# Kernel optimization log

Hardware: AMD Instinct MI355X
Metric: run time of the kernel (lower is better)

## Reference

```python
import jax, jax.numpy as jnp
import numpy as np

B, T, D = 1, 2048, 1024
H = 16
SEM_DIM, GEO_DIM, ATTN_DIM = 512, 512, 1024
ROPE_BASE = 10000.0
NEG = -1e9


def setup_inputs() -> dict:
    key = jax.random.key(0)
    ks = jax.random.split(key, 10)
    s = 0.02
    return {
        "x": jax.random.normal(ks[0], (B, T, D), jnp.float32),
        "wq_sem": jax.random.normal(ks[1], (D, SEM_DIM), jnp.float32) * s,
        "wk_sem": jax.random.normal(ks[2], (D, SEM_DIM), jnp.float32) * s,
        "wq_geo": jax.random.normal(ks[3], (D, GEO_DIM), jnp.float32) * s,
        "wk_geo": jax.random.normal(ks[4], (D, GEO_DIM), jnp.float32) * s,
        "wv": jax.random.normal(ks[5], (D, ATTN_DIM), jnp.float32) * s,
        "wo": jax.random.normal(ks[6], (ATTN_DIM, D), jnp.float32) * s,
        "k_sem_null": jax.random.normal(ks[7], (SEM_DIM,), jnp.float32) * s,
        "k_geo_null": jax.random.normal(ks[8], (GEO_DIM,), jnp.float32) * s,
        "v_null": jax.random.normal(ks[9], (ATTN_DIM,), jnp.float32) * s,
    }


def _heads(y, hd):
    b, t, _ = y.shape
    return y.reshape(b, t, H, hd).transpose(0, 2, 1, 3)  # [B,H,T,hd]


def _rope(x, cos, sin):
    # x: [B,H,T,hd], cos/sin: [T,hd//2] (rotate-half convention)
    hd = x.shape[-1]
    x1, x2 = x[..., : hd // 2], x[..., hd // 2 :]
    c = cos[None, None]
    sn = sin[None, None]
    return jnp.concatenate([x1 * c - x2 * sn, x2 * c + x1 * sn], axis=-1)


def _forward(x, wq_sem, wk_sem, wq_geo, wk_geo, wv, wo, k_sem_null, k_geo_null, v_null):
    b, t, _ = x.shape
    sem_hd = wq_sem.shape[1] // H
    geo_hd = wq_geo.shape[1] // H
    v_hd = wv.shape[1] // H
    sem_scale = 1.0 / np.sqrt(sem_hd)
    geo_scale = 1.0 / np.sqrt(geo_hd)

    qs = _heads(x @ wq_sem, sem_hd)
    ks = _heads(x @ wk_sem, sem_hd)
    qg = _heads(x @ wq_geo, geo_hd)
    kg = _heads(x @ wk_geo, geo_hd)
    v = _heads(x @ wv, v_hd)

    # RoPE on geometric branch only
    pos = jnp.arange(t, dtype=jnp.float32)
    inv_freq = 1.0 / (ROPE_BASE ** (jnp.arange(0, geo_hd, 2, dtype=jnp.float32) / geo_hd))
    ang = pos[:, None] * inv_freq[None, :]  # [T, geo_hd//2]
    cos, sin = jnp.cos(ang), jnp.sin(ang)
    qg = _rope(qg, cos, sin)
    kg = _rope(kg, cos, sin)

    # prepend null KV slot (not rotated, always attendable)
    ksn = jnp.broadcast_to(k_sem_null.reshape(1, 1, H, sem_hd).transpose(0, 2, 1, 3), (b, H, 1, sem_hd))
    kgn = jnp.broadcast_to(k_geo_null.reshape(1, 1, H, geo_hd).transpose(0, 2, 1, 3), (b, H, 1, geo_hd))
    vn = jnp.broadcast_to(v_null.reshape(1, 1, H, v_hd).transpose(0, 2, 1, 3), (b, H, 1, v_hd))
    ks_full = jnp.concatenate([ksn, ks], axis=2)  # [B,H,T+1,sem_hd]
    kg_full = jnp.concatenate([kgn, kg], axis=2)
    v_full = jnp.concatenate([vn, v], axis=2)

    # decoupled scores in fp32: sem*sem_scale + geo*geo_scale
    scores = (
        jnp.einsum("bhqd,bhkd->bhqk", qs, ks_full).astype(jnp.float32) * sem_scale
        + jnp.einsum("bhqd,bhkd->bhqk", qg, kg_full).astype(jnp.float32) * geo_scale
    )

    # causal mask over real tokens; null slot (key index 0) always visible
    causal = jnp.tril(jnp.ones((t, t), dtype=bool))
    mask = jnp.concatenate([jnp.ones((t, 1), dtype=bool), causal], axis=1)  # [T, T+1]
    scores = jnp.where(mask[None, None], scores, NEG)

    probs = jax.nn.softmax(scores, axis=-1).astype(v.dtype)
    out = jnp.einsum("bhqk,bhkd->bhqd", probs, v_full)  # [B,H,T,v_hd]
    out = out.transpose(0, 2, 1, 3).reshape(b, t, H * v_hd)
    return out @ wo


def reference(x, wq_sem, wk_sem, wq_geo, wk_geo, wv, wo, k_sem_null, k_geo_null, v_null):
    return _forward(x, wq_sem, wk_sem, wq_geo, wk_geo, wv, wo, k_sem_null, k_geo_null, v_null)
```

## Files before the change

kernel.cpp:

```cpp
#include <hip/hip_runtime.h>
#include <hip/hip_bf16.h>

typedef __hip_bfloat16 bf16;
typedef __attribute__((ext_vector_type(8))) short bf16x8;
typedef __attribute__((ext_vector_type(4))) short bf16x4;
typedef __attribute__((ext_vector_type(4))) float f32x4;

#define TSEQ   2048
#define DMODEL 1024
#define NHEAD  16
#define KST    2112
#define SCALE  0.17677669529663687f
#define LN1E4_16 0.5756462732485115f

__device__ __forceinline__ unsigned short f2bf(float f) {
    union { bf16 h; unsigned short u; } x;
    x.h = __float2bfloat16(f);
    return x.u;
}
__device__ __forceinline__ float bf2f(unsigned short u) {
    return __uint_as_float(((unsigned int)u) << 16);
}

__device__ __forceinline__ void gload_lds16(const void* g, void* l) {
    __builtin_amdgcn_global_load_lds(
        (const __attribute__((address_space(1))) void*)g,
        (__attribute__((address_space(3))) void*)l, 16, 0, 0);
}

__global__ __launch_bounds__(256) void convert_x(const float* __restrict__ X,
                                                 unsigned short* __restrict__ Xb)
{
    int i = (blockIdx.x * 256 + threadIdx.x) * 4;
    float4 v = *(const float4*)(X + i);
    ushort4 o;
    o.x = f2bf(v.x); o.y = f2bf(v.y); o.z = f2bf(v.z); o.w = f2bf(v.w);
    *(ushort4*)(Xb + i) = o;
}

__global__ __launch_bounds__(256) void transpose_all(
    const float* __restrict__ wqs, const float* __restrict__ wks,
    const float* __restrict__ wqg, const float* __restrict__ wkg,
    const float* __restrict__ wv,  const float* __restrict__ wo,
    unsigned short* __restrict__ WcatT, unsigned short* __restrict__ WoT)
{
    __shared__ float T[64][65];
    const float* src; unsigned short* dst; int C;
    switch (blockIdx.z) {
        case 0: src = wqs; dst = WcatT;               C = 512;  break;
        case 1: src = wks; dst = WcatT + 512  * 1024; C = 512;  break;
        case 2: src = wqg; dst = WcatT + 1024 * 1024; C = 512;  break;
        case 3: src = wkg; dst = WcatT + 1536 * 1024; C = 512;  break;
        case 4: src = wv;  dst = WcatT + 2048 * 1024; C = 1024; break;
        default: src = wo; dst = WoT;                 C = 1024; break;
    }
    const int c0 = blockIdx.x * 64;
    if (c0 >= C) return;
    const int r0 = blockIdx.y * 64;
    const int tid = threadIdx.x;
    #pragma unroll
    for (int i = 0; i < 16; ++i) {
        int idx = tid + 256 * i;
        int r = idx >> 6, c = idx & 63;
        T[r][c] = src[(size_t)(r0 + r) * C + c0 + c];
    }
    __syncthreads();
    #pragma unroll
    for (int i = 0; i < 16; ++i) {
        int idx = tid + 256 * i;
        int cc = idx >> 6, rr = idx & 63;
        dst[(size_t)(c0 + cc) * 1024 + r0 + rr] = f2bf(T[rr][cc]);
    }
}

__global__ __launch_bounds__(256) void init_null(
    const float* __restrict__ ksn, const float* __restrict__ kgn,
    const float* __restrict__ vn,
    unsigned short* __restrict__ Kc, unsigned short* __restrict__ Vg)
{
    const int h = blockIdx.x;
    const int tid = threadIdx.x;
    const int d = tid & 63, g = tid >> 6;
    if (g == 0)
        Kc[((size_t)h * KST + 0) * 64 + d] =
            f2bf(d < 32 ? ksn[h * 32 + d] : kgn[h * 32 + d - 32]);
    if (g == 1)
        Vg[((size_t)h * 64 + d) * KST + 0] = f2bf(vn[h * 64 + d]);
    for (int fk = 2049 + g; fk < KST; fk += 4) {
        Kc[((size_t)h * KST + fk) * 64 + d] = 0;
        Vg[((size_t)h * 64 + d) * KST + fk] = 0;
    }
}

__global__ __launch_bounds__(256) void gemm_proj_fused(
    const unsigned short* __restrict__ A,
    const unsigned short* __restrict__ Bt,
    unsigned short* __restrict__ Qc,
    unsigned short* __restrict__ Kc,
    unsigned short* __restrict__ Vg)
{
    __shared__ __align__(16) unsigned short Abuf[64 * 32];
    __shared__ __align__(16) unsigned short Bbuf[128 * 32];
    const int n0 = blockIdx.x * 128, m0 = blockIdx.y * 64;
    const int tid = threadIdx.x, l = tid & 63, wv = tid >> 6;
    const int wr = wv >> 1, wc = wv & 1;
    const int lr = l & 15, lg = l >> 4, kf = lg * 8;

    const int arow = wv * 16 + (l >> 2);
    const int aseg = (l & 3) * 8;

    f32x4 acc[2][4];
    #pragma unroll
    for (int i = 0; i < 2; ++i)
        #pragma unroll
        for (int j = 0; j < 4; ++j) acc[i][j] = (f32x4){0.f, 0.f, 0.f, 0.f};

    for (int k0 = 0; k0 < 1024; k0 += 32) {
        gload_lds16(A + (size_t)(m0 + arow) * 1024 + k0 + aseg, &Abuf[wv * 512]);
        #pragma unroll
        for (int it = 0; it < 2; ++it) {
            int brow = it * 64 + wv * 16 + (l >> 2);
            gload_lds16(Bt + (size_t)(n0 + brow) * 1024 + k0 + aseg,
                        &Bbuf[(it * 256 + wv * 64) * 8]);
        }
        __syncthreads();
        bf16x8 af[2], bfv[4];
        #pragma unroll
        for (int mf = 0; mf < 2; ++mf)
            af[mf] = *(const bf16x8*)&Abuf[(wr * 32 + mf * 16 + lr) * 32 + kf];
        #pragma unroll
        for (int nf = 0; nf < 4; ++nf)
            bfv[nf] = *(const bf16x8*)&Bbuf[(wc * 64 + nf * 16 + lr) * 32 + kf];
        #pragma unroll
        for (int mf = 0; mf < 2; ++mf)
            #pragma unroll
            for (int nf = 0; nf < 4; ++nf)
                acc[mf][nf] = __builtin_amdgcn_mfma_f32_16x16x32_bf16(
                    af[mf], bfv[nf], acc[mf][nf], 0, 0, 0);
        __syncthreads();
    }

    const int sec = n0 >> 9;
    if (sec <= 1) {
        unsigned short* dst = (sec == 0) ? Qc : Kc;
        const int tstr  = (sec == 0) ? TSEQ : KST;
        const int fkoff = (sec == 0) ? 0 : 1;
        const float sc  = (sec == 0) ? SCALE : 1.0f;
        #pragma unroll
        for (int mf = 0; mf < 2; ++mf)
            #pragma unroll
            for (int nf = 0; nf < 4; ++nf) {
                int col = (n0 & 511) + wc * 64 + nf * 16 + lr;
                int h = col >> 5, d = col & 31;
                #pragma unroll
                for (int reg = 0; reg < 4; ++reg) {
                    int q = m0 + wr * 32 + mf * 16 + lg * 4 + reg;
                    dst[((size_t)h * tstr + q + fkoff) * 64 + d] =
                        f2bf(acc[mf][nf][reg] * sc);
                }
            }
    } else if (sec <= 3) {
        unsigned short* dst = (sec == 2) ? Qc : Kc;
        const int tstr  = (sec == 2) ? TSEQ : KST;
        const int fkoff = (sec == 2) ? 0 : 1;
        const float sc  = (sec == 2) ? SCALE : 1.0f;
        const float invf = __expf(-(float)lr * LN1E4_16);
        #pragma unroll
        for (int mf = 0; mf < 2; ++mf)
            #pragma unroll
            for (int reg = 0; reg < 4; ++reg) {
                int q = m0 + wr * 32 + mf * 16 + lg * 4 + reg;
                float s, c;
                __sincosf((float)q * invf, &s, &c);
                #pragma unroll
                for (int nfp = 0; nfp < 2; ++nfp) {
                    int nf0 = nfp * 2;
                    int colbase = (n0 & 511) + wc * 64 + nf0 * 16;
                    int h = colbase >> 5;
                    float x1 = acc[mf][nf0][reg], x2 = acc[mf][nf0 + 1][reg];
                    size_t base = ((size_t)h * tstr + q + fkoff) * 64 + 32;
                    dst[base + lr]      = f2bf((x1 * c - x2 * s) * sc);
                    dst[base + lr + 16] = f2bf((x2 * c + x1 * s) * sc);
                }
            }
    } else {
        #pragma unroll
        for (int nf = 0; nf < 4; ++nf) {
            int colr = (n0 - 2048) + wc * 64 + nf * 16 + lr;
            int h = colr >> 6, dv = colr & 63;
            size_t rowbase = ((size_t)h * 64 + dv) * KST;
            #pragma unroll
            for (int mf = 0; mf < 2; ++mf)
                #pragma unroll
                for (int reg = 0; reg < 4; ++reg) {
                    int q = m0 + wr * 32 + mf * 16 + lg * 4 + reg;
                    Vg[rowbase + q + 1] = f2bf(acc[mf][nf][reg]);
                }
        }
    }
}

__global__ __launch_bounds__(256) void gemm_out(const unsigned short* __restrict__ A,
                                                const unsigned short* __restrict__ Bt,
                                                float* __restrict__ C)
{
    __shared__ __align__(16) unsigned short Abuf[64 * 32];
    __shared__ __align__(16) unsigned short Bbuf[64 * 32];
    const int n0 = blockIdx.x * 64, m0 = blockIdx.y * 64;
    const int tid = threadIdx.x, l = tid & 63, wv = tid >> 6;
    const int wr = wv >> 1, wc = wv & 1;
    const int lr = l & 15, lg = l >> 4, kf = lg * 8;

    const int arow = wv * 16 + (l >> 2);
    const int aseg = (l & 3) * 8;

    f32x4 acc[2][2];
    #pragma unroll
    for (int i = 0; i < 2; ++i)
        #pragma unroll
        for (int j = 0; j < 2; ++j) acc[i][j] = (f32x4){0.f, 0.f, 0.f, 0.f};

    for (int k0 = 0; k0 < 1024; k0 += 32) {
        gload_lds16(A  + (size_t)(m0 + arow) * 1024 + k0 + aseg, &Abuf[wv * 512]);
        gload_lds16(Bt + (size_t)(n0 + arow) * 1024 + k0 + aseg, &Bbuf[wv * 512]);
        __syncthreads();
        bf16x8 af[2], bfv[2];
        #pragma unroll
        for (int mf = 0; mf < 2; ++mf)
            af[mf] = *(const bf16x8*)&Abuf[(wr * 32 + mf * 16 + lr) * 32 + kf];
        #pragma unroll
        for (int nf = 0; nf < 2; ++nf)
            bfv[nf] = *(const bf16x8*)&Bbuf[(wc * 32 + nf * 16 + lr) * 32 + kf];
        #pragma unroll
        for (int mf = 0; mf < 2; ++mf)
            #pragma unroll
            for (int nf = 0; nf < 2; ++nf)
                acc[mf][nf] = __builtin_amdgcn_mfma_f32_16x16x32_bf16(
                    af[mf], bfv[nf], acc[mf][nf], 0, 0, 0);
        __syncthreads();
    }
    #pragma unroll
    for (int mf = 0; mf < 2; ++mf)
        #pragma unroll
        for (int nf = 0; nf < 2; ++nf)
            #pragma unroll
            for (int reg = 0; reg < 4; ++reg) {
                int row = m0 + wr * 32 + mf * 16 + lg * 4 + reg;
                int col = n0 + wc * 32 + nf * 16 + lr;
                C[(size_t)row * DMODEL + col] = acc[mf][nf][reg];
            }
}

__global__ __launch_bounds__(256) void attn_mfma(
    const unsigned short* __restrict__ Qc,
    const unsigned short* __restrict__ Kc,
    const unsigned short* __restrict__ Vg,
    unsigned short* __restrict__ attnO,
    unsigned short* __restrict__ OpA,
    unsigned short* __restrict__ OpB,
    float2* __restrict__ ml)
{
    __shared__ __align__(16) unsigned short KsL[2][64 * 64];
    __shared__ __align__(16) unsigned short VsL[2][64 * 64];
    __shared__ __align__(16) unsigned short Ps[64 * 64];

    const int h = blockIdx.y;
    int qb, part, np;
    {
        int i = blockIdx.x;
        if (i < 24)      { np = 4; qb = 31 - (i >> 2); part = i & 3; }
        else if (i < 51) { int j = i - 24; np = 3; qb = 25 - j / 3; part = j % 3; }
        else if (i < 69) { int j = i - 51; np = 2; qb = 16 - (j >> 1); part = j & 1; }
        else             { np = 1; qb = 7 - (blockIdx.x - 69); part = 0; }
    }
    const int nt = qb + 2;
    const int base = nt / np, rem = nt % np;
    const int t0 = part * base + (part < rem ? part : rem);
    const int t1 = t0 + base + (part < rem ? 1 : 0);

    const int q0 = qb * 64;
    const int tid = threadIdx.x, l = tid & 63, w = tid >> 6;
    const int lr = l & 15, lg = l >> 4;

    const int qrow = q0 + w * 16 + lr;
    bf16x8 qa0 = *(const bf16x8*)&Qc[((size_t)h * TSEQ + qrow) * 64 + lg * 8];
    bf16x8 qa1 = *(const bf16x8*)&Qc[((size_t)h * TSEQ + qrow) * 64 + 32 + lg * 8];

    const int sc8 = (((l & 7) ^ ((l >> 3) & 7))) * 8;
    const int r0s = (w * 2 + 0) * 8 + (l >> 3);
    const int r1s = (w * 2 + 1) * 8 + (l >> 3);
    const unsigned short* Kh = Kc + (((size_t)h * KST) << 6);
    const unsigned short* Vh = Vg + (size_t)h * 64 * KST;

#define STAGE_KV(bufi, fk0_) do {                                              \
        gload_lds16(Kh + (((size_t)((fk0_) + r0s)) << 6) + sc8,                \
                    &KsL[bufi][(w * 2 + 0) * 512]);                            \
        gload_lds16(Kh + (((size_t)((fk0_) + r1s)) << 6) + sc8,                \
                    &KsL[bufi][(w * 2 + 1) * 512]);                            \
        gload_lds16(Vh + (size_t)r0s * KST + (fk0_) + sc8,                     \
                    &VsL[bufi][(w * 2 + 0) * 512]);                            \
        gload_lds16(Vh + (size_t)r1s * KST + (fk0_) + sc8,                     \
                    &VsL[bufi][(w * 2 + 1) * 512]);                            \
    } while (0)

    f32x4 o[4];
    #pragma unroll
    for (int i = 0; i < 4; ++i) o[i] = (f32x4){0.f, 0.f, 0.f, 0.f};
    float m = -1e30f, ll = 0.0f;
    const int q = qrow;

    int buf = 0;
    STAGE_KV(0, t0 * 64);
    asm volatile("s_waitcnt vmcnt(0)" ::: "memory");
    __builtin_amdgcn_s_barrier();

    for (int kb = t0; kb < t1; ++kb) {
        const int fk0 = kb * 64;
        if (kb + 1 < t1) STAGE_KV(buf ^ 1, fk0 + 64);

        const unsigned short* Ksb = &KsL[buf][0];
        const unsigned short* Vsb = &VsL[buf][0];

        f32x4 sa[4];
        #pragma unroll
        for (int i = 0; i < 4; ++i) sa[i] = (f32x4){0.f, 0.f, 0.f, 0.f};
        __builtin_amdgcn_s_setprio(1);
        #pragma unroll
        for (int ks = 0; ks < 2; ++ks) {
            int dd = lg * 8 + ks * 32;
            bf16x8 qa = ks ? qa1 : qa0;
            #pragma unroll
            for (int nf = 0; nf < 4; ++nf) {
                int kkc = nf * 16 + lr;
                bf16x8 kbf = *(const bf16x8*)&Ksb[kkc * 64 + (dd ^ ((kkc & 7) << 3))];
                sa[nf] = __builtin_amdgcn_mfma_f32_16x16x32_bf16(kbf, qa, sa[nf], 0, 0, 0);
            }
        }
        __builtin_amdgcn_s_setprio(0);

        float sv[4][4];
        float mt = -1e30f;
        #pragma unroll
        for (int nf = 0; nf < 4; ++nf)
            #pragma unroll
            for (int reg = 0; reg < 4; ++reg) {
                int fk = fk0 + nf * 16 + lg * 4 + reg;
                float val = (fk <= q + 1) ? sa[nf][reg] : -1e9f;
                sv[nf][reg] = val;
                mt = fmaxf(mt, val);
            }
        mt = fmaxf(mt, __shfl_xor(mt, 16, 64));
        mt = fmaxf(mt, __shfl_xor(mt, 32, 64));
        if (__any(mt > m + 8.0f)) {
            float mn = fmaxf(m, mt);
            float alpha = __expf(m - mn);
            m = mn;
            ll *= alpha;
            #pragma unroll
            for (int nf = 0; nf < 4; ++nf)
                #pragma unroll
                for (int reg = 0; reg < 4; ++reg)
                    o[nf][reg] *= alpha;
        }
        float rs = 0.0f;
        #pragma unroll
        for (int nf = 0; nf < 4; ++nf)
            #pragma unroll
            for (int reg = 0; reg < 4; ++reg) {
                float p = __expf(sv[nf][reg] - m);
                sv[nf][reg] = p;
                rs += p;
            }
        rs += __shfl_xor(rs, 16, 64);
        rs += __shfl_xor(rs, 32, 64);
        ll += rs;

        {
            int r = w * 16 + lr;
            #pragma unroll
            for (int nf = 0; nf < 4; ++nf) {
                bf16x4 pk;
                pk[0] = f2bf(sv[nf][0]); pk[1] = f2bf(sv[nf][1]);
                pk[2] = f2bf(sv[nf][2]); pk[3] = f2bf(sv[nf][3]);
                int kk0 = nf * 16 + lg * 4;
                *(bf16x4*)&Ps[r * 64 + (kk0 ^ ((r & 7) << 3))] = pk;
            }
        }

        __builtin_amdgcn_s_setprio(1);
        #pragma unroll
        for (int ks = 0; ks < 2; ++ks) {
            int kk0 = lg * 8 + ks * 32;
            int pr  = w * 16 + lr;
            bf16x8 pa = *(const bf16x8*)&Ps[pr * 64 + (kk0 ^ ((pr & 7) << 3))];
            #pragma unroll
            for (int nf = 0; nf < 4; ++nf) {
                int dv = nf * 16 + lr;
                bf16x8 vb = *(const bf16x8*)&Vsb[dv * 64 + (kk0 ^ ((dv & 7) << 3))];
                o[nf] = __builtin_amdgcn_mfma_f32_16x16x32_bf16(vb, pa, o[nf], 0, 0, 0);
            }
        }
        __builtin_amdgcn_s_setprio(0);

        asm volatile("s_waitcnt vmcnt(0)" ::: "memory");
        __builtin_amdgcn_s_barrier();
        buf ^= 1;
    }
#undef STAGE_KV

    const float inv = 1.0f / ll;
    if (np == 1) {
        #pragma unroll
        for (int nf = 0; nf < 4; ++nf)
            #pragma unroll
            for (int reg = 0; reg < 4; ++reg) {
                int dv = nf * 16 + lg * 4 + reg;
                attnO[(size_t)q * DMODEL + h * 64 + dv] = f2bf(o[nf][reg] * inv);
            }
    } else {
        const int sidx = h * 69 + blockIdx.x;
        unsigned short* Od = (sidx < 768)
            ? OpA + (size_t)sidx * 4096
            : OpB + (size_t)(sidx - 768) * 4096;
        const int r = w * 16 + lr;
        #pragma unroll
        for (int nf = 0; nf < 4; ++nf)
            #pragma unroll
            for (int reg = 0; reg < 4; ++reg) {
                int dv = nf * 16 + lg * 4 + reg;
                Od[r * 64 + dv] = f2bf(o[nf][reg] * inv);
            }
        if (lg == 0)
            ml[sidx * 64 + r] = make_float2(m, ll);
    }
}

__global__ __launch_bounds__(256) void combine_wave(
    const unsigned short* __restrict__ OpA,
    const unsigned short* __restrict__ OpB,
    const float2* __restrict__ ml,
    unsigned short* __restrict__ attnO)
{
    const int qb = 8 + blockIdx.x;
    const int h  = blockIdx.y;
    int np, i0;
    if (qb >= 26)      { np = 4; i0 = (31 - qb) * 4; }
    else if (qb >= 17) { np = 3; i0 = 24 + (25 - qb) * 3; }
    else               { np = 2; i0 = 51 + (16 - qb) * 2; }
    const int sidx0 = h * 69 + i0;

    const int t = threadIdx.x;
    const int r = t >> 2, dv0 = (t & 3) * 16;

    float wt[4];
    float mm = -1e30f;
    #pragma unroll
    for (int p = 0; p < 4; ++p) {
        wt[p] = 0.0f;
        if (p < np) {
            float2 v = ml[(sidx0 + p) * 64 + r];
            wt[p] = v.x;
            mm = fmaxf(mm, v.x);
        }
    }
    float tot = 0.0f;
    #pragma unroll
    for (int p = 0; p < 4; ++p) {
        if (p < np) {
            float2 v = ml[(sidx0 + p) * 64 + r];
            wt[p] = v.y * __expf(v.x - mm);
            tot += wt[p];
        }
    }
    const float inv = 1.0f / tot;

    float accv[16];
    #pragma unroll
    for (int c = 0; c < 16; ++c) accv[c] = 0.0f;
    #pragma unroll
    for (int p = 0; p < 4; ++p) {
        if (p < np) {
            int s = sidx0 + p;
            const unsigned short* Od = (s < 768)
                ? OpA + (size_t)s * 4096
                : OpB + (size_t)(s - 768) * 4096;
            #pragma unroll
            for (int c4 = 0; c4 < 4; ++c4) {
                ushort4 v = *(const ushort4*)&Od[r * 64 + dv0 + c4 * 4];
                accv[c4 * 4 + 0] += wt[p] * bf2f(v.x);
                accv[c4 * 4 + 1] += wt[p] * bf2f(v.y);
                accv[c4 * 4 + 2] += wt[p] * bf2f(v.z);
                accv[c4 * 4 + 3] += wt[p] * bf2f(v.w);
            }
        }
    }
    const int q = qb * 64 + r;
    #pragma unroll
    for (int c4 = 0; c4 < 4; ++c4) {
        ushort4 ov;
        ov.x = f2bf(accv[c4 * 4 + 0] * inv);
        ov.y = f2bf(accv[c4 * 4 + 1] * inv);
        ov.z = f2bf(accv[c4 * 4 + 2] * inv);
        ov.w = f2bf(accv[c4 * 4 + 3] * inv);
        *(ushort4*)&attnO[(size_t)q * DMODEL + h * 64 + dv0 + c4 * 4] = ov;
    }
}

extern "C" void kernel_launch(void* const* d_in, const int* in_sizes, int n_in,
                              void* d_out, int out_size, void* d_ws, size_t ws_size,
                              hipStream_t stream)
{
    const float* x      = (const float*)d_in[0];
    const float* wq_sem = (const float*)d_in[1];
    const float* wk_sem = (const float*)d_in[2];
    const float* wq_geo = (const float*)d_in[3];
    const float* wk_geo = (const float*)d_in[4];
    const float* wv     = (const float*)d_in[5];
    const float* wo     = (const float*)d_in[6];
    const float* ksn    = (const float*)d_in[7];
    const float* kgn    = (const float*)d_in[8];
    const float* vn     = (const float*)d_in[9];
    float* out = (float*)d_out;

    char* ws = (char*)d_ws;
    unsigned short* Xb    = (unsigned short*)(ws);
    unsigned short* attnO = (unsigned short*)(ws);
    unsigned short* WcatT = (unsigned short*)(ws + 4194304);
    unsigned short* OpA   = (unsigned short*)(ws + 4194304);
    unsigned short* WoT   = (unsigned short*)(ws + 10485760);
    unsigned short* Qc    = (unsigned short*)(ws + 12582912);
    unsigned short* Kc    = (unsigned short*)(ws + 16777216);
    unsigned short* Vg    = (unsigned short*)(ws + 21102592);
    unsigned short* OpB   = (unsigned short*)(ws + 25427968);
    float2*         ml    = (float2*)(ws + 28180480);

    convert_x<<<2048, 256, 0, stream>>>(x, Xb);
    transpose_all<<<dim3(16, 16, 6), 256, 0, stream>>>(
        wq_sem, wk_sem, wq_geo, wk_geo, wv, wo, WcatT, WoT);
    init_null<<<16, 256, 0, stream>>>(ksn, kgn, vn, Kc, Vg);

    gemm_proj_fused<<<dim3(24, 32), 256, 0, stream>>>(Xb, WcatT, Qc, Kc, Vg);

    attn_mfma<<<dim3(77, NHEAD), 256, 0, stream>>>(Qc, Kc, Vg, attnO, OpA, OpB, ml);
    combine_wave<<<dim3(24, NHEAD), 256, 0, stream>>>(OpA, OpB, ml, attnO);

    gemm_out<<<dim3(16, 32), 256, 0, stream>>>(attnO, WoT, out);
}
```

Baseline: 95.32 us.

## Use 128-row query tiles in attention and merge prep kernels into one launch

Attention blocks now cover 128 query rows instead of 64, with each wave computing two 16-row groups against the same K/V tile held in LDS. This halves K/V staging per query row and doubles MFMA work per LDS read. The split-K partition table, partial-output layout, and combine kernel are resized to match. Full causal-mask evaluation is skipped for tiles entirely below the diagonal, and the three preprocessing kernels are merged into a single launch. The trade-off is more register pressure and fewer blocks in the grid.

```diff
diff --git a/kernel.cpp b/kernel.cpp
--- a/kernel.cpp
+++ b/kernel.cpp
@@ -28,67 +28,67 @@
         (__attribute__((address_space(3))) void*)l, 16, 0, 0);
 }
 
-__global__ __launch_bounds__(256) void convert_x(const float* __restrict__ X,
-                                                 unsigned short* __restrict__ Xb)
-{
-    int i = (blockIdx.x * 256 + threadIdx.x) * 4;
-    float4 v = *(const float4*)(X + i);
-    ushort4 o;
-    o.x = f2bf(v.x); o.y = f2bf(v.y); o.z = f2bf(v.z); o.w = f2bf(v.w);
-    *(ushort4*)(Xb + i) = o;
-}
-
-__global__ __launch_bounds__(256) void transpose_all(
+__global__ __launch_bounds__(256) void prep_all(
+    const float* __restrict__ X,
     const float* __restrict__ wqs, const float* __restrict__ wks,
     const float* __restrict__ wqg, const float* __restrict__ wkg,
     const float* __restrict__ wv,  const float* __restrict__ wo,
-    unsigned short* __restrict__ WcatT, unsigned short* __restrict__ WoT)
+    const float* __restrict__ ksn, const float* __restrict__ kgn,
+    const float* __restrict__ vn,
+    unsigned short* __restrict__ Xb,
+    unsigned short* __restrict__ WcatT, unsigned short* __restrict__ WoT,
+    unsigned short* __restrict__ Kc, unsigned short* __restrict__ Vg)
 {
     __shared__ float T[64][65];
-    const float* src; unsigned short* dst; int C;
-    switch (blockIdx.z) {
-        case 0: src = wqs; dst = WcatT;               C = 512;  break;
-        case 1: src = wks; dst = WcatT + 512  * 1024; C = 512;  break;
-        case 2: src = wqg; dst = WcatT + 1024 * 1024; C = 512;  break;
-        case 3: src = wkg; dst = WcatT + 1536 * 1024; C = 512;  break;
-        case 4: src = wv;  dst = WcatT + 2048 * 1024; C = 1024; break;
-        default: src = wo; dst = WoT;                 C = 1024; break;
-    }
-    const int c0 = blockIdx.x * 64;
-    if (c0 >= C) return;
-    const int r0 = blockIdx.y * 64;
+    const int bx = blockIdx.x;
     const int tid = threadIdx.x;
-    #pragma unroll
-    for (int i = 0; i < 16; ++i) {
-        int idx = tid + 256 * i;
-        int r = idx >> 6, c = idx & 63;
-        T[r][c] = src[(size_t)(r0 + r) * C + c0 + c];
-    }
-    __syncthreads();
-    #pragma unroll
-    for (int i = 0; i < 16; ++i) {
-        int idx = tid + 256 * i;
-        int cc = idx >> 6, rr = idx & 63;
-        dst[(size_t)(c0 + cc) * 1024 + r0 + rr] = f2bf(T[rr][cc]);
-    }
-}
-
-__global__ __launch_bounds__(256) void init_null(
-    const float* __restrict__ ksn, const float* __restrict__ kgn,
-    const float* __restrict__ vn,
-    unsigned short* __restrict__ Kc, unsigned short* __restrict__ Vg)
-{
-    const int h = blockIdx.x;
-    const int tid = threadIdx.x;
-    const int d = tid & 63, g = tid >> 6;
-    if (g == 0)
-        Kc[((size_t)h * KST + 0) * 64 + d] =
-            f2bf(d < 32 ? ksn[h * 32 + d] : kgn[h * 32 + d - 32]);
-    if (g == 1)
-        Vg[((size_t)h * 64 + d) * KST + 0] = f2bf(vn[h * 64 + d]);
-    for (int fk = 2049 + g; fk < KST; fk += 4) {
-        Kc[((size_t)h * KST + fk) * 64 + d] = 0;
-        Vg[((size_t)h * 64 + d) * KST + fk] = 0;
+    if (bx < 2048) {
+        int i = (bx * 256 + tid) * 4;
+        float4 v = *(const float4*)(X + i);
+        ushort4 o;
+        o.x = f2bf(v.x); o.y = f2bf(v.y); o.z = f2bf(v.z); o.w = f2bf(v.w);
+        *(ushort4*)(Xb + i) = o;
+    } else if (bx < 3584) {
+        const int idx = bx - 2048;
+        const int z = idx >> 8, rem = idx & 255;
+        const int cx = rem & 15, ry = rem >> 4;
+        const float* src; unsigned short* dst; int C;
+        switch (z) {
+            case 0: src = wqs; dst = WcatT;               C = 512;  break;
+            case 1: src = wks; dst = WcatT + 512  * 1024; C = 512;  break;
+            case 2: src = wqg; dst = WcatT + 1024 * 1024; C = 512;  break;
+            case 3: src = wkg; dst = WcatT + 1536 * 1024; C = 512;  break;
+            case 4: src = wv;  dst = WcatT + 2048 * 1024; C = 1024; break;
+            default: src = wo; dst = WoT;                 C = 1024; break;
+        }
+        const int c0 = cx * 64;
+        if (c0 >= C) return;
+        const int r0 = ry * 64;
+        #pragma unroll
+        for (int i = 0; i < 16; ++i) {
+            int id2 = tid + 256 * i;
+            int r = id2 >> 6, c = id2 & 63;
+            T[r][c] = src[(size_t)(r0 + r) * C + c0 + c];
+        }
+        __syncthreads();
+        #pragma unroll
+        for (int i = 0; i < 16; ++i) {
+            int id2 = tid + 256 * i;
+            int cc = id2 >> 6, rr = id2 & 63;
+            dst[(size_t)(c0 + cc) * 1024 + r0 + rr] = f2bf(T[rr][cc]);
+        }
+    } else {
+        const int h = bx - 3584;
+        const int d = tid & 63, g = tid >> 6;
+        if (g == 0)
+            Kc[((size_t)h * KST + 0) * 64 + d] =
+                f2bf(d < 32 ? ksn[h * 32 + d] : kgn[h * 32 + d - 32]);
+        if (g == 1)
+            Vg[((size_t)h * 64 + d) * KST + 0] = f2bf(vn[h * 64 + d]);
+        for (int fk = 2049 + g; fk < KST; fk += 4) {
+            Kc[((size_t)h * KST + fk) * 64 + d] = 0;
+            Vg[((size_t)h * 64 + d) * KST + fk] = 0;
+        }
     }
 }
 
@@ -262,29 +262,33 @@
 {
     __shared__ __align__(16) unsigned short KsL[2][64 * 64];
     __shared__ __align__(16) unsigned short VsL[2][64 * 64];
-    __shared__ __align__(16) unsigned short Ps[64 * 64];
+    __shared__ __align__(16) unsigned short Ps[128 * 64];
 
     const int h = blockIdx.y;
     int qb, part, np;
     {
         int i = blockIdx.x;
-        if (i < 24)      { np = 4; qb = 31 - (i >> 2); part = i & 3; }
-        else if (i < 51) { int j = i - 24; np = 3; qb = 25 - j / 3; part = j % 3; }
-        else if (i < 69) { int j = i - 51; np = 2; qb = 16 - (j >> 1); part = j & 1; }
-        else             { np = 1; qb = 7 - (blockIdx.x - 69); part = 0; }
-    }
-    const int nt = qb + 2;
-    const int base = nt / np, rem = nt % np;
-    const int t0 = part * base + (part < rem ? part : rem);
-    const int t1 = t0 + base + (part < rem ? 1 : 0);
-
-    const int q0 = qb * 64;
+        if (i < 16)      { np = 4; qb = 15 - (i >> 2); part = i & 3; }
+        else if (i < 28) { int j = i - 16; np = 3; qb = 11 - j / 3; part = j % 3; }
+        else if (i < 38) { int j = i - 28; np = 2; qb = 7 - (j >> 1); part = j & 1; }
+        else             { np = 1; qb = 2 - (blockIdx.x - 38); part = 0; }
+    }
+    const int nt = 2 * qb + 3;
+    const int bsz = nt / np, rem = nt % np;
+    const int t0 = part * bsz + (part < rem ? part : rem);
+    const int t1 = t0 + bsz + (part < rem ? 1 : 0);
+
+    const int q0 = qb * 128;
     const int tid = threadIdx.x, l = tid & 63, w = tid >> 6;
     const int lr = l & 15, lg = l >> 4;
 
-    const int qrow = q0 + w * 16 + lr;
-    bf16x8 qa0 = *(const bf16x8*)&Qc[((size_t)h * TSEQ + qrow) * 64 + lg * 8];
-    bf16x8 qa1 = *(const bf16x8*)&Qc[((size_t)h * TSEQ + qrow) * 64 + 32 + lg * 8];
+    bf16x8 qa[2][2];
+    #pragma unroll
+    for (int rg = 0; rg < 2; ++rg) {
+        int qr = q0 + w * 32 + rg * 16 + lr;
+        qa[rg][0] = *(const bf16x8*)&Qc[((size_t)h * TSEQ + qr) * 64 + lg * 8];
+        qa[rg][1] = *(const bf16x8*)&Qc[((size_t)h * TSEQ + qr) * 64 + 32 + lg * 8];
+    }
 
     const int sc8 = (((l & 7) ^ ((l >> 3) & 7))) * 8;
     const int r0s = (w * 2 + 0) * 8 + (l >> 3);
@@ -303,11 +307,13 @@
                     &VsL[bufi][(w * 2 + 1) * 512]);                            \
     } while (0)
 
-    f32x4 o[4];
-    #pragma unroll
-    for (int i = 0; i < 4; ++i) o[i] = (f32x4){0.f, 0.f, 0.f, 0.f};
-    float m = -1e30f, ll = 0.0f;
-    const int q = qrow;
+    f32x4 o[2][4];
+    #pragma unroll
+    for (int rg = 0; rg < 2; ++rg)
+        #pragma unroll
+        for (int i = 0; i < 4; ++i) o[rg][i] = (f32x4){0.f, 0.f, 0.f, 0.f};
+    float m[2]  = {-1e30f, -1e30f};
+    float ll[2] = {0.f, 0.f};
 
     int buf = 0;
     STAGE_KV(0, t0 * 64);
@@ -321,67 +327,79 @@
         const unsigned short* Ksb = &KsL[buf][0];
         const unsigned short* Vsb = &VsL[buf][0];
 
-        f32x4 sa[4];
-        #pragma unroll
-        for (int i = 0; i < 4; ++i) sa[i] = (f32x4){0.f, 0.f, 0.f, 0.f};
+        f32x4 sa[2][4];
+        #pragma unroll
+        for (int rg = 0; rg < 2; ++rg)
+            #pragma unroll
+            for (int i = 0; i < 4; ++i) sa[rg][i] = (f32x4){0.f, 0.f, 0.f, 0.f};
         __builtin_amdgcn_s_setprio(1);
         #pragma unroll
         for (int ks = 0; ks < 2; ++ks) {
             int dd = lg * 8 + ks * 32;
-            bf16x8 qa = ks ? qa1 : qa0;
             #pragma unroll
             for (int nf = 0; nf < 4; ++nf) {
                 int kkc = nf * 16 + lr;
                 bf16x8 kbf = *(const bf16x8*)&Ksb[kkc * 64 + (dd ^ ((kkc & 7) << 3))];
-                sa[nf] = __builtin_amdgcn_mfma_f32_16x16x32_bf16(kbf, qa, sa[nf], 0, 0, 0);
+                sa[0][nf] = __builtin_amdgcn_mfma_f32_16x16x32_bf16(kbf, qa[0][ks], sa[0][nf], 0, 0, 0);
+                sa[1][nf] = __builtin_amdgcn_mfma_f32_16x16x32_bf16(kbf, qa[1][ks], sa[1][nf], 0, 0, 0);
             }
         }
         __builtin_amdgcn_s_setprio(0);
 
-        float sv[4][4];
-        float mt = -1e30f;
-        #pragma unroll
-        for (int nf = 0; nf < 4; ++nf)
-            #pragma unroll
-            for (int reg = 0; reg < 4; ++reg) {
-                int fk = fk0 + nf * 16 + lg * 4 + reg;
-                float val = (fk <= q + 1) ? sa[nf][reg] : -1e9f;
-                sv[nf][reg] = val;
-                mt = fmaxf(mt, val);
-            }
-        mt = fmaxf(mt, __shfl_xor(mt, 16, 64));
-        mt = fmaxf(mt, __shfl_xor(mt, 32, 64));
-        if (__any(mt > m + 8.0f)) {
-            float mn = fmaxf(m, mt);
-            float alpha = __expf(m - mn);
-            m = mn;
-            ll *= alpha;
+        const bool needmask = (fk0 + 62 > q0 + w * 32);
+        #pragma unroll
+        for (int rg = 0; rg < 2; ++rg) {
+            const int q = q0 + w * 32 + rg * 16 + lr;
+            float mt = -1e30f;
+            if (needmask) {
+                #pragma unroll
+                for (int nf = 0; nf < 4; ++nf)
+                    #pragma unroll
+                    for (int reg = 0; reg < 4; ++reg) {
+                        int fk = fk0 + nf * 16 + lg * 4 + reg;
+                        float val = (fk <= q + 1) ? sa[rg][nf][reg] : -1e9f;
+                        sa[rg][nf][reg] = val;
+                        mt = fmaxf(mt, val);
+                    }
+            } else {
+                #pragma unroll
+                for (int nf = 0; nf < 4; ++nf)
+                    #pragma unroll
+                    for (int reg = 0; reg < 4; ++reg)
+                        mt = fmaxf(mt, sa[rg][nf][reg]);
+            }
+            mt = fmaxf(mt, __shfl_xor(mt, 16, 64));
+            mt = fmaxf(mt, __shfl_xor(mt, 32, 64));
+            if (__any(mt > m[rg] + 8.0f)) {
+                float mn = fmaxf(m[rg], mt);
+                float alpha = __expf(m[rg] - mn);
+                m[rg] = mn;
+                ll[rg] *= alpha;
+                #pragma unroll
+                for (int nf = 0; nf < 4; ++nf)
+                    #pragma unroll
+                    for (int reg = 0; reg < 4; ++reg)
+                        o[rg][nf][reg] *= alpha;
+            }
+            float rs = 0.0f;
             #pragma unroll
             for (int nf = 0; nf < 4; ++nf)
                 #pragma unroll
-                for (int reg = 0; reg < 4; ++reg)
-                    o[nf][reg] *= alpha;
-        }
-        float rs = 0.0f;
-        #pragma unroll
-        for (int nf = 0; nf < 4; ++nf)
-            #pragma unroll
-            for (int reg = 0; reg < 4; ++reg) {
-                float p = __expf(sv[nf][reg] - m);
-                sv[nf][reg] = p;
-                rs += p;
-            }
-        rs += __shfl_xor(rs, 16, 64);
-        rs += __shfl_xor(rs, 32, 64);
-        ll += rs;
-
-        {
-            int r = w * 16 + lr;
+                for (int reg = 0; reg < 4; ++reg) {
+                    float p = __expf(sa[rg][nf][reg] - m[rg]);
+                    sa[rg][nf][reg] = p;
+                    rs += p;
+                }
+            rs += __shfl_xor(rs, 16, 64);
+            rs += __shfl_xor(rs, 32, 64);
+            ll[rg] += rs;
+
+            int r = w * 32 + rg * 16 + lr;
             #pragma unroll
             for (int nf = 0; nf < 4; ++nf) {
                 bf16x4 pk;
-                pk[0] = f2bf(sv[nf][0]); pk[1] = f2bf(sv[nf][1]);
-                pk[2] = f2bf(sv[nf][2]); pk[3] = f2bf(sv[nf][3]);
+                pk[0] = f2bf(sa[rg][nf][0]); pk[1] = f2bf(sa[rg][nf][1]);
+                pk[2] = f2bf(sa[rg][nf][2]); pk[3] = f2bf(sa[rg][nf][3]);
                 int kk0 = nf * 16 + lg * 4;
                 *(bf16x4*)&Ps[r * 64 + (kk0 ^ ((r & 7) << 3))] = pk;
             }
@@ -391,13 +409,15 @@
         #pragma unroll
         for (int ks = 0; ks < 2; ++ks) {
             int kk0 = lg * 8 + ks * 32;
-            int pr  = w * 16 + lr;
-            bf16x8 pa = *(const bf16x8*)&Ps[pr * 64 + (kk0 ^ ((pr & 7) << 3))];
+            int swz = kk0 ^ ((lr & 7) << 3);
+            bf16x8 pa0 = *(const bf16x8*)&Ps[(w * 32 + lr) * 64 + swz];
+            bf16x8 pa1 = *(const bf16x8*)&Ps[(w * 32 + 16 + lr) * 64 + swz];
             #pragma unroll
             for (int nf = 0; nf < 4; ++nf) {
                 int dv = nf * 16 + lr;
                 bf16x8 vb = *(const bf16x8*)&Vsb[dv * 64 + (kk0 ^ ((dv & 7) << 3))];
-                o[nf] = __builtin_amdgcn_mfma_f32_16x16x32_bf16(vb, pa, o[nf], 0, 0, 0);
+                o[0][nf] = __builtin_amdgcn_mfma_f32_16x16x32_bf16(vb, pa0, o[0][nf], 0, 0, 0);
+                o[1][nf] = __builtin_amdgcn_mfma_f32_16x16x32_bf16(vb, pa1, o[1][nf], 0, 0, 0);
             }
         }
         __builtin_amdgcn_s_setprio(0);
@@ -408,30 +428,34 @@
     }
 #undef STAGE_KV
 
-    const float inv = 1.0f / ll;
-    if (np == 1) {
-        #pragma unroll
-        for (int nf = 0; nf < 4; ++nf)
-            #pragma unroll
-            for (int reg = 0; reg < 4; ++reg) {
-                int dv = nf * 16 + lg * 4 + reg;
-                attnO[(size_t)q * DMODEL + h * 64 + dv] = f2bf(o[nf][reg] * inv);
-            }
-    } else {
-        const int sidx = h * 69 + blockIdx.x;
-        unsigned short* Od = (sidx < 768)
-            ? OpA + (size_t)sidx * 4096
-            : OpB + (size_t)(sidx - 768) * 4096;
-        const int r = w * 16 + lr;
-        #pragma unroll
-        for (int nf = 0; nf < 4; ++nf)
-            #pragma unroll
-            for (int reg = 0; reg < 4; ++reg) {
-                int dv = nf * 16 + lg * 4 + reg;
-                Od[r * 64 + dv] = f2bf(o[nf][reg] * inv);
-            }
-        if (lg == 0)
-            ml[sidx * 64 + r] = make_float2(m, ll);
+    const int sidx = h * 38 + blockIdx.x;
+    unsigned short* Od = (np == 1) ? 0
+        : ((sidx < 384) ? OpA + (size_t)sidx * 8192
+                        : OpB + (size_t)(sidx - 384) * 8192);
+    #pragma unroll
+    for (int rg = 0; rg < 2; ++rg) {
+        const float inv = 1.0f / ll[rg];
+        const int q = q0 + w * 32 + rg * 16 + lr;
+        if (np == 1) {
+            #pragma unroll
+            for (int nf = 0; nf < 4; ++nf) {
+                ushort4 ov;
+                ov.x = f2bf(o[rg][nf][0] * inv); ov.y = f2bf(o[rg][nf][1] * inv);
+                ov.z = f2bf(o[rg][nf][2] * inv); ov.w = f2bf(o[rg][nf][3] * inv);
+                *(ushort4*)&attnO[(size_t)q * DMODEL + h * 64 + nf * 16 + lg * 4] = ov;
+            }
+        } else {
+            const int r = w * 32 + rg * 16 + lr;
+            #pragma unroll
+            for (int nf = 0; nf < 4; ++nf) {
+                ushort4 ov;
+                ov.x = f2bf(o[rg][nf][0] * inv); ov.y = f2bf(o[rg][nf][1] * inv);
+                ov.z = f2bf(o[rg][nf][2] * inv); ov.w = f2bf(o[rg][nf][3] * inv);
+                *(ushort4*)&Od[r * 64 + nf * 16 + lg * 4] = ov;
+            }
+            if (lg == 0)
+                ml[sidx * 128 + r] = make_float2(m[rg], ll[rg]);
+        }
     }
 }
 
@@ -441,51 +465,46 @@
     const float2* __restrict__ ml,
     unsigned short* __restrict__ attnO)
 {
-    const int qb = 8 + blockIdx.x;
+    const int qb = 3 + blockIdx.x;
     const int h  = blockIdx.y;
     int np, i0;
-    if (qb >= 26)      { np = 4; i0 = (31 - qb) * 4; }
-    else if (qb >= 17) { np = 3; i0 = 24 + (25 - qb) * 3; }
-    else               { np = 2; i0 = 51 + (16 - qb) * 2; }
-    const int sidx0 = h * 69 + i0;
+    if (qb >= 12)     { np = 4; i0 = (15 - qb) * 4; }
+    else if (qb >= 8) { np = 3; i0 = 16 + (11 - qb) * 3; }
+    else              { np = 2; i0 = 28 + (7 - qb) * 2; }
+    const int sidx0 = h * 38 + i0;
 
     const int t = threadIdx.x;
-    const int r = t >> 2, dv0 = (t & 3) * 16;
+    const int r = t & 127, dv0 = (t >> 7) * 32;
 
     float wt[4];
     float mm = -1e30f;
+    #pragma unroll
+    for (int p = 0; p < 4; ++p)
+        if (p < np) mm = fmaxf(mm, ml[(sidx0 + p) * 128 + r].x);
+    float tot = 0.0f;
     #pragma unroll
     for (int p = 0; p < 4; ++p) {
         wt[p] = 0.0f;
         if (p < np) {
-            float2 v = ml[(sidx0 + p) * 64 + r];
-            wt[p] = v.x;
-            mm = fmaxf(mm, v.x);
-        }
-    }
-    float tot = 0.0f;
-    #pragma unroll
-    for (int p = 0; p < 4; ++p) {
-        if (p < np) {
-            float2 v = ml[(sidx0 + p) * 64 + r];
+            float2 v = ml[(sidx0 + p) * 128 + r];
             wt[p] = v.y * __expf(v.x - mm);
             tot += wt[p];
         }
     }
     const float inv = 1.0f / tot;
 
-    float accv[16];
-    #pragma unroll
-    for (int c = 0; c < 16; ++c) accv[c] = 0.0f;
+    float accv[32];
+    #pragma unroll
+    for (int c = 0; c < 32; ++c) accv[c] = 0.0f;
     #pragma unroll
     for (int p = 0; p < 4; ++p) {
         if (p < np) {
             int s = sidx0 + p;
-            const unsigned short* Od = (s < 768)
-                ? OpA + (size_t)s * 4096
-                : OpB + (size_t)(s - 768) * 4096;
-            #pragma unroll
-            for (int c4 = 0; c4 < 4; ++c4) {
+            const unsigned short* Od = (s < 384)
+                ? OpA + (size_t)s * 8192
+                : OpB + (size_t)(s - 384) * 8192;
+            #pragma unroll
+            for (int c4 = 0; c4 < 8; ++c4) {
                 ushort4 v = *(const ushort4*)&Od[r * 64 + dv0 + c4 * 4];
                 accv[c4 * 4 + 0] += wt[p] * bf2f(v.x);
                 accv[c4 * 4 + 1] += wt[p] * bf2f(v.y);
@@ -494,9 +513,9 @@
             }
         }
     }
-    const int q = qb * 64 + r;
-    #pragma unroll
-    for (int c4 = 0; c4 < 4; ++c4) {
+    const int q = qb * 128 + r;
+    #pragma unroll
+    for (int c4 = 0; c4 < 8; ++c4) {
         ushort4 ov;
         ov.x = f2bf(accv[c4 * 4 + 0] * inv);
         ov.y = f2bf(accv[c4 * 4 + 1] * inv);
@@ -532,17 +551,15 @@
     unsigned short* Kc    = (unsigned short*)(ws + 16777216);
     unsigned short* Vg    = (unsigned short*)(ws + 21102592);
     unsigned short* OpB   = (unsigned short*)(ws + 25427968);
-    float2*         ml    = (float2*)(ws + 28180480);
-
-    convert_x<<<2048, 256, 0, stream>>>(x, Xb);
-    transpose_all<<<dim3(16, 16, 6), 256, 0, stream>>>(
-        wq_sem, wk_sem, wq_geo, wk_geo, wv, wo, WcatT, WoT);
-    init_null<<<16, 256, 0, stream>>>(ksn, kgn, vn, Kc, Vg);
+    float2*         ml    = (float2*)(ws + 29097984);
+
+    prep_all<<<3600, 256, 0, stream>>>(x, wq_sem, wk_sem, wq_geo, wk_geo, wv, wo,
+                                       ksn, kgn, vn, Xb, WcatT, WoT, Kc, Vg);
 
     gemm_proj_fused<<<dim3(24, 32), 256, 0, stream>>>(Xb, WcatT, Qc, Kc, Vg);
 
-    attn_mfma<<<dim3(77, NHEAD), 256, 0, stream>>>(Qc, Kc, Vg, attnO, OpA, OpB, ml);
-    combine_wave<<<dim3(24, NHEAD), 256, 0, stream>>>(OpA, OpB, ml, attnO);
+    attn_mfma<<<dim3(41, NHEAD), 256, 0, stream>>>(Qc, Kc, Vg, attnO, OpA, OpB, ml);
+    combine_wave<<<dim3(13, NHEAD), 256, 0, stream>>>(OpA, OpB, ml, attnO);
 
     gemm_out<<<dim3(16, 32), 256, 0, stream>>>(attnO, WoT, out);
 }
```

Measured after the change: 96.48 us. Within noise of the previous version (+1.2%).
